# Performance work log

Measured on AMD Instinct MI355X. Metric: run time of the kernel, lower is better.

The kernel has to match this reference:

```python
import jax, jax.numpy as jnp
import numpy as np

N = 100000   # nodes
E = 3200000  # edges per graph
D = 16       # embedding_size, num_heads = 1
ATTN_SLOPE = 0.2   # DGL GATv2Conv negative_slope default
ACT_SLOPE = 0.01   # torch.nn.functional.leaky_relu default (activation arg)


def gatv2_layer(h, src, dst, W_src, b_src, W_dst, b_dst, attn):
    """DGL GATv2Conv with num_heads=1, activation=leaky_relu.
    h: [N, D]; src/dst: [E] int; W_*: [D, D]; b_*: [D]; attn: [D].
    """
    feat_src = h @ W_src + b_src          # [N, D]
    feat_dst = h @ W_dst + b_dst          # [N, D]
    el = feat_src[src]                    # [E, D] gather to edges
    e = jax.nn.leaky_relu(el + feat_dst[dst], ATTN_SLOPE)  # [E, D]
    score = e @ attn                      # [E] attention logits
    # segment softmax over incoming edges of each destination node
    smax = jax.ops.segment_max(score, dst, num_segments=N)
    smax = jnp.where(jnp.isfinite(smax), smax, 0.0)  # empty segments -> 0
    ex = jnp.exp(score - smax[dst])       # [E]
    denom = jax.ops.segment_sum(ex, dst, num_segments=N)  # [N]
    alpha = ex / denom[dst]               # [E]
    rst = jax.ops.segment_sum(alpha[:, None] * el, dst, num_segments=N)  # [N, D]
    return jax.nn.leaky_relu(rst, ACT_SLOPE)


def setup_inputs() -> dict:
    key = jax.random.key(0)
    ks = jax.random.split(key, 16)
    s = 1.0 / np.sqrt(D)
    return {
        "embedding": jax.random.normal(ks[0], (N, D), jnp.float32),
        "src1": jax.random.randint(ks[1], (E,), 0, N, jnp.int32),
        "dst1": jax.random.randint(ks[2], (E,), 0, N, jnp.int32),
        "src2": jax.random.randint(ks[3], (E,), 0, N, jnp.int32),
        "dst2": jax.random.randint(ks[4], (E,), 0, N, jnp.int32),
        "W_src1": jax.random.normal(ks[5], (D, D), jnp.float32) * s,
        "b_src1": jnp.zeros((D,), jnp.float32),
        "W_dst1": jax.random.normal(ks[6], (D, D), jnp.float32) * s,
        "b_dst1": jnp.zeros((D,), jnp.float32),
        "attn1": jax.random.normal(ks[7], (D,), jnp.float32) * s,
        "W_src2": jax.random.normal(ks[8], (D, D), jnp.float32) * s,
        "b_src2": jnp.zeros((D,), jnp.float32),
        "W_dst2": jax.random.normal(ks[9], (D, D), jnp.float32) * s,
        "b_dst2": jnp.zeros((D,), jnp.float32),
        "attn2": jax.random.normal(ks[10], (D,), jnp.float32) * s,
    }


def reference(embedding, src1, dst1, src2, dst2,
              W_src1, b_src1, W_dst1, b_dst1, attn1,
              W_src2, b_src2, W_dst2, b_dst2, attn2):
    user2item = gatv2_layer(embedding, src1, dst1, W_src1, b_src1, W_dst1, b_dst1, attn1)
    item_influence = gatv2_layer(user2item, src2, dst2, W_src2, b_src2, W_dst2, b_dst2, attn2)
    return item_influence  # [N, D]
```

## Files before the change

kernel.cpp:

```cpp
#include <hip/hip_runtime.h>
#include <hip/hip_fp16.h>

#define D 16
#define R 64
#define RBITS 6
#define RMASK 63
#define STRIDE 2560
#define CAP 2560
#define ACCT 512
#define KPT (CAP / ACCT)
#define EPB 16384
#define CHK 8192
#define K1T 1024
#define NB2 1664
#define ATTN_SLOPE 0.2f
#define ACT_SLOPE 0.01f

__device__ __forceinline__ float leaky_a(float v) {
    return v > 0.f ? v : ATTN_SLOPE * v;
}
__device__ __forceinline__ float2 h2f(unsigned u) {
    __half2 h = *(__half2*)&u;
    return __half22float2(h);
}


__device__ void binscatter_tile(int tile, const int* __restrict__ src,
                                const int* __restrict__ dst,
                                int* __restrict__ gcur, unsigned* __restrict__ binned,
                                int E, int NB, char* sb) {
    unsigned* sorted = (unsigned*)sb;
    unsigned short* sposb = (unsigned short*)(sb + 32768);
    int* soffs = (int*)(sb + 49152);
    int* wcur = (int*)(sb + 49152 + 4 * NB2);
    int* swsum = (int*)(sb + 49152 + 8 * NB2);
    int tid = threadIdx.x;
    int lane = tid & 63, w = tid >> 6;
    int base = tile * EPB;
    int count = E - base;
    if (count > EPB) count = EPB;

    for (int i = tid; i < NB; i += K1T) wcur[i] = 0;
    __syncthreads();

    if (count == EPB) {
        const int4* d4 = (const int4*)(dst + base);
#pragma unroll
        for (int m = 0; m < 4; m++) {
            int4 a = d4[m * K1T + tid];
            atomicAdd(&wcur[a.x >> RBITS], 1);
            atomicAdd(&wcur[a.y >> RBITS], 1);
            atomicAdd(&wcur[a.z >> RBITS], 1);
            atomicAdd(&wcur[a.w >> RBITS], 1);
        }
    } else {
        for (int k = 0; k < 16; k++) {
            int e = base + k * K1T + tid;
            if (e < E) atomicAdd(&wcur[dst[e] >> RBITS], 1);
        }
    }
    __syncthreads();

    for (int i = tid; i < NB; i += K1T) {
        int c = wcur[i];
        if (c > 0) {
            int res = atomicAdd(&gcur[i], c);
            wcur[i] = i * STRIDE + res;
        }
    }
    __syncthreads();

    int i0 = 2 * tid, i1 = 2 * tid + 1;
    for (int c = 0; c < 2; c++) {
        int cbase = base + c * CHK;
        int cc = count - c * CHK;
        if (cc <= 0) break;
        if (cc > CHK) cc = CHK;
        bool full = (cc == CHK);

        for (int i = tid; i < NB; i += K1T) soffs[i] = 0;
        __syncthreads();

        if (full) {
            const int4* d4 = (const int4*)(dst + cbase);
            int4 a = d4[tid], b4 = d4[K1T + tid];
            atomicAdd(&soffs[a.x >> RBITS], 1);
            atomicAdd(&soffs[a.y >> RBITS], 1);
            atomicAdd(&soffs[a.z >> RBITS], 1);
            atomicAdd(&soffs[a.w >> RBITS], 1);
            atomicAdd(&soffs[b4.x >> RBITS], 1);
            atomicAdd(&soffs[b4.y >> RBITS], 1);
            atomicAdd(&soffs[b4.z >> RBITS], 1);
            atomicAdd(&soffs[b4.w >> RBITS], 1);
        } else {
            for (int k = 0; k < 8; k++) {
                int e = cbase + k * K1T + tid;
                if (e < E) atomicAdd(&soffs[dst[e] >> RBITS], 1);
            }
        }
        __syncthreads();

        int a0 = (i0 < NB) ? soffs[i0] : 0;
        int a1 = (i1 < NB) ? soffs[i1] : 0;
        int pair = a0 + a1;
        int x = pair;
#pragma unroll
        for (int ofs = 1; ofs < 64; ofs <<= 1) {
            int y = __shfl_up(x, ofs, 64);
            if (lane >= ofs) x += y;
        }
        if (lane == 63) swsum[w] = x;
        __syncthreads();
        if (w == 0) {
            int v = (lane < 16) ? swsum[lane] : 0;
            int s = v;
#pragma unroll
            for (int ofs = 1; ofs < 16; ofs <<= 1) {
                int y = __shfl_up(s, ofs, 64);
                if (lane >= ofs) s += y;
            }
            if (lane < 16) swsum[lane] = s - v;
        }
        __syncthreads();
        int excl = x - pair + swsum[w];
        int e0 = excl, e1 = excl + a0;
        int d0v = 0, d1v = 0;
        if (i0 < NB) {
            soffs[i0] = e0;
            if (a0 > 0) { d0v = wcur[i0] - e0; wcur[i0] = d0v; }
        }
        if (i1 < NB) {
            soffs[i1] = e1;
            if (a1 > 0) { d1v = wcur[i1] - e1; wcur[i1] = d1v; }
        }
        __syncthreads();

        if (full) {
            const int4* d4 = (const int4*)(dst + cbase);
            const int4* s4 = (const int4*)(src + cbase);
            int4 a = d4[tid], b4 = d4[K1T + tid];
            int4 sa = s4[tid], sb4 = s4[K1T + tid];
            int dd[8] = {a.x, a.y, a.z, a.w, b4.x, b4.y, b4.z, b4.w};
            int ss[8] = {sa.x, sa.y, sa.z, sa.w, sb4.x, sb4.y, sb4.z, sb4.w};
#pragma unroll
            for (int m = 0; m < 8; m++) {
                int bb = dd[m] >> RBITS;
                int r = atomicAdd(&soffs[bb], 1);
                sorted[r] = ((unsigned)ss[m] << RBITS) | (unsigned)(dd[m] & RMASK);
                sposb[r] = (unsigned short)bb;
            }
        } else {
            for (int k = 0; k < 8; k++) {
                int e = cbase + k * K1T + tid;
                if (e < E) {
                    int dv = dst[e];
                    int bb = dv >> RBITS;
                    int r = atomicAdd(&soffs[bb], 1);
                    sorted[r] = ((unsigned)src[e] << RBITS) | (unsigned)(dv & RMASK);
                    sposb[r] = (unsigned short)bb;
                }
            }
        }
        __syncthreads();

#pragma unroll
        for (int m = 0; m < 8; m++) {
            int p = m * K1T + tid;
            if (p < cc) {
                int bb = sposb[p];
                int pos = p + wcur[bb];
                if (pos < (bb + 1) * STRIDE) binned[pos] = sorted[p];
            }
        }
        __syncthreads();

        if (c == 0) {
            if (i0 < NB && a0 > 0) wcur[i0] = d0v + e0 + a0;
            if (i1 < NB && a1 > 0) wcur[i1] = d1v + e1 + a1;
            __syncthreads();
        }
    }
}

__device__ void transform_tile(int tile, const float* __restrict__ h,
                               const float* __restrict__ Ws, const float* __restrict__ bs,
                               const float* __restrict__ Wd, const float* __restrict__ bd,
                               __half* __restrict__ fsh, float* __restrict__ fdst,
                               int N, char* sb) {
    float* sWs = (float*)sb;
    float* sWd = sWs + 256;
    float* sbs = sWd + 256;
    float* sbd = sbs + 16;
    int t = threadIdx.x;
    if (t < 256) { sWs[t] = Ws[t]; sWd[t] = Wd[t]; }
    if (t < 16) { sbs[t] = bs[t]; sbd[t] = bd[t]; }
    __syncthreads();
    int n = tile * K1T + t;
    if (n >= N) return;
    float hv[D];
    const float4* h4 = (const float4*)(h + (size_t)n * D);
#pragma unroll
    for (int k = 0; k < 4; k++) {
        float4 v = h4[k];
        hv[4 * k] = v.x; hv[4 * k + 1] = v.y; hv[4 * k + 2] = v.z; hv[4 * k + 3] = v.w;
    }
    float os[D], od[D];
#pragma unroll
    for (int d = 0; d < D; d++) {
        float ss = sbs[d];
        float sd = sbd[d];
#pragma unroll
        for (int k = 0; k < D; k++) {
            ss += hv[k] * sWs[k * D + d];
            sd += hv[k] * sWd[k * D + d];
        }
        os[d] = ss; od[d] = sd;
    }
    unsigned us[8];
#pragma unroll
    for (int k = 0; k < 8; k++) {
        __half2 hh = __floats2half2_rn(os[2 * k], os[2 * k + 1]);
        us[k] = *(unsigned*)&hh;
    }
    uint4* fo = (uint4*)(fsh + (size_t)n * D);
    fo[0] = make_uint4(us[0], us[1], us[2], us[3]);
    fo[1] = make_uint4(us[4], us[5], us[6], us[7]);
    float4* fd4 = (float4*)(fdst + (size_t)n * D);
#pragma unroll
    for (int k = 0; k < 4; k++)
        fd4[k] = make_float4(od[4 * k], od[4 * k + 1], od[4 * k + 2], od[4 * k + 3]);
}

__global__ void __launch_bounds__(K1T)
k1_kernel(const float* h, const float* Ws, const float* bs,
          const float* Wd, const float* bd,
          __half* fsh, float* fdst,
          const int* srcA, const int* dstA, int* gA, unsigned* binnedA, int EA,
          const int* srcB, const int* dstB, int* gB, unsigned* binnedB, int EB,
          int N, int NB, int B1, int B2, int TT) {
    __shared__ __align__(16) char sb[49152 + 8 * NB2 + 64];
    int bid = blockIdx.x;
    if (bid < B1) {
        binscatter_tile(bid, srcA, dstA, gA, binnedA, EA, NB, sb);
    } else if (bid < B1 + B2) {
        binscatter_tile(bid - B1, srcB, dstB, gB, binnedB, EB, NB, sb);
    } else {
        int t = bid - B1 - B2;
        if (t < TT) transform_tile(t, h, Ws, bs, Wd, bd, fsh, fdst, N, sb);
    }
}


template <bool DO_TAIL>
__global__ void __launch_bounds__(ACCT)
acc_kernel(const unsigned* __restrict__ binned, const int* __restrict__ gcur,
           const __half* __restrict__ fsh, const float* __restrict__ fdst,
           const float* __restrict__ attn, float* __restrict__ out,
           __half* __restrict__ fs2h, float* __restrict__ fd2,
           const float* __restrict__ Ws2, const float* __restrict__ bs2,
           const float* __restrict__ Wd2, const float* __restrict__ bd2,
           int N) {
    __shared__ float sfd[R * D];
    __shared__ int ebuf[CAP];
    __shared__ float exbuf[CAP];
    __shared__ int cstart[R + 1];
    __shared__ int cur[R];
    __shared__ float wtail[544];
    int b = blockIdx.x;
    int tid = threadIdx.x;
    int node0 = b * R;
    int nn = N - node0;
    if (nn > R) nn = R;
    for (int i = tid; i < nn * D; i += ACCT) sfd[i] = fdst[node0 * D + i];
    if (tid <= R) cstart[tid] = 0;
    if (DO_TAIL) {
        if (tid < 256) { wtail[tid] = Ws2[tid]; wtail[256 + tid] = Wd2[tid]; }
        if (tid < 16) { wtail[512 + tid] = bs2[tid]; wtail[528 + tid] = bd2[tid]; }
    }

    float av[D];
#pragma unroll
    for (int k = 0; k < D; k++) av[k] = attn[k];

    int cnt = gcur[b];
    if (cnt > CAP) cnt = CAP;
    int base = b * STRIDE;

    unsigned pls[KPT];
#pragma unroll
    for (int k = 0; k < KPT; k++) {
        int j = k * ACCT + tid;
        pls[k] = (j < cnt) ? binned[base + j] : 0xFFFFFFFFu;
    }
    __syncthreads();

    const uint4* fsh4 = (const uint4*)fsh;
    const uint2* fsq = (const uint2*)fsh;
    const float4* sfd4 = (const float4*)sfd;

#pragma unroll
    for (int k = 0; k < KPT; k++)
        if (pls[k] != 0xFFFFFFFFu) atomicAdd(&cstart[pls[k] & RMASK], 1);

    float exs[KPT];
#pragma unroll
    for (int k = 0; k + 1 < KPT; k += 2) {
        unsigned q0 = pls[k], q1 = pls[k + 1];
        uint4 ua0, ub0, ua1, ub1;
        if (q0 != 0xFFFFFFFFu) {
            int s = q0 >> RBITS;
            ua0 = fsh4[2 * s]; ub0 = fsh4[2 * s + 1];
        }
        if (q1 != 0xFFFFFFFFu) {
            int s = q1 >> RBITS;
            ua1 = fsh4[2 * s]; ub1 = fsh4[2 * s + 1];
        }
        if (q0 != 0xFFFFFFFFu) {
            int loc = q0 & RMASK;
            float4 f0 = sfd4[loc * 4 + 0], f1 = sfd4[loc * 4 + 1];
            float4 f2 = sfd4[loc * 4 + 2], f3 = sfd4[loc * 4 + 3];
            float2 c0 = h2f(ua0.x), c1 = h2f(ua0.y), c2 = h2f(ua0.z), c3 = h2f(ua0.w);
            float2 c4 = h2f(ub0.x), c5 = h2f(ub0.y), c6 = h2f(ub0.z), c7 = h2f(ub0.w);
            float p = leaky_a(c0.x + f0.x) * av[0]  + leaky_a(c0.y + f0.y) * av[1]
                    + leaky_a(c1.x + f0.z) * av[2]  + leaky_a(c1.y + f0.w) * av[3]
                    + leaky_a(c2.x + f1.x) * av[4]  + leaky_a(c2.y + f1.y) * av[5]
                    + leaky_a(c3.x + f1.z) * av[6]  + leaky_a(c3.y + f1.w) * av[7]
                    + leaky_a(c4.x + f2.x) * av[8]  + leaky_a(c4.y + f2.y) * av[9]
                    + leaky_a(c5.x + f2.z) * av[10] + leaky_a(c5.y + f2.w) * av[11]
                    + leaky_a(c6.x + f3.x) * av[12] + leaky_a(c6.y + f3.y) * av[13]
                    + leaky_a(c7.x + f3.z) * av[14] + leaky_a(c7.y + f3.w) * av[15];
            exs[k] = __expf(p);
        }
        if (q1 != 0xFFFFFFFFu) {
            int loc = q1 & RMASK;
            float4 f0 = sfd4[loc * 4 + 0], f1 = sfd4[loc * 4 + 1];
            float4 f2 = sfd4[loc * 4 + 2], f3 = sfd4[loc * 4 + 3];
            float2 c0 = h2f(ua1.x), c1 = h2f(ua1.y), c2 = h2f(ua1.z), c3 = h2f(ua1.w);
            float2 c4 = h2f(ub1.x), c5 = h2f(ub1.y), c6 = h2f(ub1.z), c7 = h2f(ub1.w);
            float p = leaky_a(c0.x + f0.x) * av[0]  + leaky_a(c0.y + f0.y) * av[1]
                    + leaky_a(c1.x + f0.z) * av[2]  + leaky_a(c1.y + f0.w) * av[3]
                    + leaky_a(c2.x + f1.x) * av[4]  + leaky_a(c2.y + f1.y) * av[5]
                    + leaky_a(c3.x + f1.z) * av[6]  + leaky_a(c3.y + f1.w) * av[7]
                    + leaky_a(c4.x + f2.x) * av[8]  + leaky_a(c4.y + f2.y) * av[9]
                    + leaky_a(c5.x + f2.z) * av[10] + leaky_a(c5.y + f2.w) * av[11]
                    + leaky_a(c6.x + f3.x) * av[12] + leaky_a(c6.y + f3.y) * av[13]
                    + leaky_a(c7.x + f3.z) * av[14] + leaky_a(c7.y + f3.w) * av[15];
            exs[k + 1] = __expf(p);
        }
    }
    if (KPT & 1) {
        unsigned q0 = pls[KPT - 1];
        if (q0 != 0xFFFFFFFFu) {
            int s = q0 >> RBITS;
            uint4 ua0 = fsh4[2 * s], ub0 = fsh4[2 * s + 1];
            int loc = q0 & RMASK;
            float4 f0 = sfd4[loc * 4 + 0], f1 = sfd4[loc * 4 + 1];
            float4 f2 = sfd4[loc * 4 + 2], f3 = sfd4[loc * 4 + 3];
            float2 c0 = h2f(ua0.x), c1 = h2f(ua0.y), c2 = h2f(ua0.z), c3 = h2f(ua0.w);
            float2 c4 = h2f(ub0.x), c5 = h2f(ub0.y), c6 = h2f(ub0.z), c7 = h2f(ub0.w);
            float p = leaky_a(c0.x + f0.x) * av[0]  + leaky_a(c0.y + f0.y) * av[1]
                    + leaky_a(c1.x + f0.z) * av[2]  + leaky_a(c1.y + f0.w) * av[3]
                    + leaky_a(c2.x + f1.x) * av[4]  + leaky_a(c2.y + f1.y) * av[5]
                    + leaky_a(c3.x + f1.z) * av[6]  + leaky_a(c3.y + f1.w) * av[7]
                    + leaky_a(c4.x + f2.x) * av[8]  + leaky_a(c4.y + f2.y) * av[9]
                    + leaky_a(c5.x + f2.z) * av[10] + leaky_a(c5.y + f2.w) * av[11]
                    + leaky_a(c6.x + f3.x) * av[12] + leaky_a(c6.y + f3.y) * av[13]
                    + leaky_a(c7.x + f3.z) * av[14] + leaky_a(c7.y + f3.w) * av[15];
            exs[KPT - 1] = __expf(p);
        }
    }
    __syncthreads();
    if (tid < R) {
        int v = cstart[tid];
        int x = v;
#pragma unroll
        for (int ofs = 1; ofs < 64; ofs <<= 1) {
            int y = __shfl_up(x, ofs, 64);
            if (tid >= ofs) x += y;
        }
        cstart[tid] = x - v;
        cur[tid] = x - v;
        if (tid == R - 1) cstart[R] = x;
    }
    __syncthreads();
#pragma unroll
    for (int k = 0; k < KPT; k++) {
        unsigned pl = pls[k];
        if (pl != 0xFFFFFFFFu) {
            int r = atomicAdd(&cur[pl & RMASK], 1);
            ebuf[r] = (int)pl;
            exbuf[r] = exs[k];
        }
    }
    __syncthreads();

    int lane = tid & 63;
    int w = tid >> 6;
    int q = lane & 3;
    int s2 = (lane >> 2) & 3;
    int n2 = lane >> 4;

    float4 acc[2];
    float den[2];
#pragma unroll
    for (int i = 0; i < 2; i++) {
        acc[i] = make_float4(0.f, 0.f, 0.f, 0.f);
        den[i] = 0.f;
    }
#pragma unroll
    for (int i = 0; i < 2; i++) {
        int loc = w * 8 + i * 4 + n2;
        int kb = cstart[loc], ke = cstart[loc + 1];
        int k = kb + s2;
        for (; k + 12 < ke; k += 16) {
            int pl0 = ebuf[k];
            int pl1 = ebuf[k + 4];
            int pl2 = ebuf[k + 8];
            int pl3 = ebuf[k + 12];
            float ex0 = exbuf[k];
            float ex1 = exbuf[k + 4];
            float ex2 = exbuf[k + 8];
            float ex3 = exbuf[k + 12];
            uint2 u0 = fsq[(((unsigned)pl0) >> RBITS) * 4 + q];
            uint2 u1 = fsq[(((unsigned)pl1) >> RBITS) * 4 + q];
            uint2 u2 = fsq[(((unsigned)pl2) >> RBITS) * 4 + q];
            uint2 u3 = fsq[(((unsigned)pl3) >> RBITS) * 4 + q];
            float2 a01 = h2f(u0.x), a23 = h2f(u0.y);
            float2 b01 = h2f(u1.x), b23 = h2f(u1.y);
            float2 c01 = h2f(u2.x), c23 = h2f(u2.y);
            float2 d01 = h2f(u3.x), d23 = h2f(u3.y);
            acc[i].x += ex0 * a01.x + ex1 * b01.x + ex2 * c01.x + ex3 * d01.x;
            acc[i].y += ex0 * a01.y + ex1 * b01.y + ex2 * c01.y + ex3 * d01.y;
            acc[i].z += ex0 * a23.x + ex1 * b23.x + ex2 * c23.x + ex3 * d23.x;
            acc[i].w += ex0 * a23.y + ex1 * b23.y + ex2 * c23.y + ex3 * d23.y;
            den[i] += (ex0 + ex1) + (ex2 + ex3);
        }
        for (; k < ke; k += 4) {
            int pl = ebuf[k];
            float ex = exbuf[k];
            uint2 u = fsq[(((unsigned)pl) >> RBITS) * 4 + q];
            float2 a01 = h2f(u.x), a23 = h2f(u.y);
            acc[i].x += ex * a01.x;
            acc[i].y += ex * a01.y;
            acc[i].z += ex * a23.x;
            acc[i].w += ex * a23.y;
            den[i] += ex;
        }
    }
#pragma unroll
    for (int i = 0; i < 2; i++) {
        float4 a = acc[i];
        float dn = den[i];
#pragma unroll
        for (int m = 4; m <= 8; m <<= 1) {
            a.x += __shfl_xor(a.x, m, 16);
            a.y += __shfl_xor(a.y, m, 16);
            a.z += __shfl_xor(a.z, m, 16);
            a.w += __shfl_xor(a.w, m, 16);
            dn += __shfl_xor(dn, m, 16);
        }
        int loc = w * 8 + i * 4 + n2;
        if (s2 == 0 && loc < nn) {
            float inv = dn > 0.f ? 1.f / dn : 0.f;
            float4 v;
            v.x = a.x * inv; v.x = v.x > 0.f ? v.x : ACT_SLOPE * v.x;
            v.y = a.y * inv; v.y = v.y > 0.f ? v.y : ACT_SLOPE * v.y;
            v.z = a.z * inv; v.z = v.z > 0.f ? v.z : ACT_SLOPE * v.z;
            v.w = a.w * inv; v.w = v.w > 0.f ? v.w : ACT_SLOPE * v.w;
            if (DO_TAIL) {
                *(float4*)&sfd[loc * D + q * 4] = v;
            } else {
                ((float4*)out)[(size_t)(node0 + loc) * 4 + q] = v;
            }
        }
    }
    if (DO_TAIL) {
        __syncthreads();
        int loc = tid >> 2, qq = tid & 3;
        if (tid < 256 && loc < nn) {
            float hvv[16];
#pragma unroll
            for (int k = 0; k < 16; k++) hvv[k] = sfd[loc * D + k];
            float s0 = wtail[512 + 4 * qq], s1 = wtail[513 + 4 * qq];
            float s2v = wtail[514 + 4 * qq], s3 = wtail[515 + 4 * qq];
            float d0 = wtail[528 + 4 * qq], d1 = wtail[529 + 4 * qq];
            float d2v = wtail[530 + 4 * qq], d3 = wtail[531 + 4 * qq];
#pragma unroll
            for (int k = 0; k < 16; k++) {
                float hk = hvv[k];
                const float* wr = &wtail[k * 16 + 4 * qq];
                const float* wr2 = &wtail[256 + k * 16 + 4 * qq];
                s0 += hk * wr[0]; s1 += hk * wr[1]; s2v += hk * wr[2]; s3 += hk * wr[3];
                d0 += hk * wr2[0]; d1 += hk * wr2[1]; d2v += hk * wr2[2]; d3 += hk * wr2[3];
            }
            __half2 p0 = __floats2half2_rn(s0, s1), p1 = __floats2half2_rn(s2v, s3);
            *(uint2*)(fs2h + (size_t)(node0 + loc) * D + 4 * qq) =
                make_uint2(*(unsigned*)&p0, *(unsigned*)&p1);
            *(float4*)(fd2 + (size_t)(node0 + loc) * D + 4 * qq) =
                make_float4(d0, d1, d2v, d3);
        }
    }
}


extern "C" void kernel_launch(void* const* d_in, const int* in_sizes, int n_in,
                              void* d_out, int out_size, void* d_ws, size_t ws_size,
                              hipStream_t stream) {
    const float* emb = (const float*)d_in[0];
    const int* src1 = (const int*)d_in[1];
    const int* dst1 = (const int*)d_in[2];
    const int* src2 = (const int*)d_in[3];
    const int* dst2 = (const int*)d_in[4];
    const float* Wsrc1 = (const float*)d_in[5];
    const float* bsrc1 = (const float*)d_in[6];
    const float* Wdst1 = (const float*)d_in[7];
    const float* bdst1 = (const float*)d_in[8];
    const float* attn1 = (const float*)d_in[9];
    const float* Wsrc2 = (const float*)d_in[10];
    const float* bsrc2 = (const float*)d_in[11];
    const float* Wdst2 = (const float*)d_in[12];
    const float* bdst2 = (const float*)d_in[13];
    const float* attn2 = (const float*)d_in[14];

    const int N = in_sizes[0] / D;
    const int E1 = in_sizes[1];
    const int E2 = in_sizes[3];
    const int NB = (N + R - 1) / R;
    const size_t ndf = (size_t)N * D;

    float* ws = (float*)d_ws;
    float* fd1 = ws;
    float* fd2 = fd1 + ndf;
    __half* fs1h = (__half*)(fd2 + ndf);
    __half* fs2h = fs1h + ndf;
    int* gA = (int*)(fs2h + ndf);
    int* gB = gA + NB2;
    unsigned* binned1 = (unsigned*)(gB + NB2);
    unsigned* binned2big = binned1 + (size_t)NB * STRIDE;
    size_t bigNeed = (size_t)((char*)(binned2big + (size_t)NB * STRIDE) - (char*)d_ws);
    bool big = ws_size >= bigNeed;
    (void)n_in; (void)out_size;

    const int B1 = (E1 + EPB - 1) / EPB;
    const int B2 = (E2 + EPB - 1) / EPB;
    const int TT = (N + K1T - 1) / K1T;

    (void)hipMemsetAsync(gA, 0, 2 * NB2 * sizeof(int), stream);

    if (big) {
        k1_kernel<<<B1 + B2 + TT, K1T, 0, stream>>>(
            emb, Wsrc1, bsrc1, Wdst1, bdst1, fs1h, fd1,
            src1, dst1, gA, binned1, E1,
            src2, dst2, gB, binned2big, E2,
            N, NB, B1, B2, TT);
        acc_kernel<true><<<NB, ACCT, 0, stream>>>(
            binned1, gA, fs1h, fd1, attn1, nullptr,
            fs2h, fd2, Wsrc2, bsrc2, Wdst2, bdst2, N);
        acc_kernel<false><<<NB, ACCT, 0, stream>>>(
            binned2big, gB, fs2h, fd2, attn2, (float*)d_out,
            nullptr, nullptr, nullptr, nullptr, nullptr, nullptr, N);
    } else {
        k1_kernel<<<B1 + TT, K1T, 0, stream>>>(
            emb, Wsrc1, bsrc1, Wdst1, bdst1, fs1h, fd1,
            src1, dst1, gA, binned1, E1,
            src2, dst2, gB, binned1, 0,
            N, NB, B1, 0, TT);
        acc_kernel<true><<<NB, ACCT, 0, stream>>>(
            binned1, gA, fs1h, fd1, attn1, nullptr,
            fs2h, fd2, Wsrc2, bsrc2, Wdst2, bdst2, N);
        k1_kernel<<<B2, K1T, 0, stream>>>(
            emb, Wsrc1, bsrc1, Wdst1, bdst1, fs1h, fd1,
            src2, dst2, gB, binned1, E2,
            src2, dst2, gB, binned1, 0,
            N, NB, B2, 0, 0);
        acc_kernel<false><<<NB, ACCT, 0, stream>>>(
            binned1, gB, fs2h, fd2, attn2, (float*)d_out,
            nullptr, nullptr, nullptr, nullptr, nullptr, nullptr, N);
    }
}
```

Baseline: 235.2 us.

## Replace per-node edge sort with shared-memory atomic accumulation of weighted features

The accumulation kernel no longer builds per-destination edge lists in shared memory (counting, prefix scan, scatter, then a second gather pass). Each thread now computes the softmax weight for its edges and adds the weighted source features plus the weight directly into a padded 17-float per-node accumulator using shared-memory float atomics. The score loop is also software-pipelined to prefetch the next edge's source features. This removes the second global gather and several block barriers, but adds 17 shared atomics per edge that contend when many edges share a destination, and makes the summation order nondeterministic.

```diff
diff --git a/kernel.cpp b/kernel.cpp
--- a/kernel.cpp
+++ b/kernel.cpp
@@ -13,6 +13,7 @@
 #define CHK 8192
 #define K1T 1024
 #define NB2 1664
+#define NW 17
 #define ATTN_SLOPE 0.2f
 #define ACT_SLOPE 0.01f
 
@@ -261,10 +262,7 @@
            const float* __restrict__ Wd2, const float* __restrict__ bd2,
            int N) {
     __shared__ float sfd[R * D];
-    __shared__ int ebuf[CAP];
-    __shared__ float exbuf[CAP];
-    __shared__ int cstart[R + 1];
-    __shared__ int cur[R];
+    __shared__ float num[R * NW];
     __shared__ float wtail[544];
     int b = blockIdx.x;
     int tid = threadIdx.x;
@@ -272,7 +270,7 @@
     int nn = N - node0;
     if (nn > R) nn = R;
     for (int i = tid; i < nn * D; i += ACCT) sfd[i] = fdst[node0 * D + i];
-    if (tid <= R) cstart[tid] = 0;
+    for (int i = tid; i < R * NW; i += ACCT) num[i] = 0.f;
     if (DO_TAIL) {
         if (tid < 256) { wtail[tid] = Ws2[tid]; wtail[256 + tid] = Wd2[tid]; }
         if (tid < 16) { wtail[512 + tid] = bs2[tid]; wtail[528 + tid] = bd2[tid]; }
@@ -295,32 +293,28 @@
     __syncthreads();
 
     const uint4* fsh4 = (const uint4*)fsh;
-    const uint2* fsq = (const uint2*)fsh;
     const float4* sfd4 = (const float4*)sfd;
 
-#pragma unroll
-    for (int k = 0; k < KPT; k++)
-        if (pls[k] != 0xFFFFFFFFu) atomicAdd(&cstart[pls[k] & RMASK], 1);
-
-    float exs[KPT];
-#pragma unroll
-    for (int k = 0; k + 1 < KPT; k += 2) {
-        unsigned q0 = pls[k], q1 = pls[k + 1];
-        uint4 ua0, ub0, ua1, ub1;
-        if (q0 != 0xFFFFFFFFu) {
-            int s = q0 >> RBITS;
-            ua0 = fsh4[2 * s]; ub0 = fsh4[2 * s + 1];
-        }
-        if (q1 != 0xFFFFFFFFu) {
-            int s = q1 >> RBITS;
-            ua1 = fsh4[2 * s]; ub1 = fsh4[2 * s + 1];
-        }
-        if (q0 != 0xFFFFFFFFu) {
-            int loc = q0 & RMASK;
+    unsigned qc = pls[0];
+    uint4 ua, ub;
+    if (qc != 0xFFFFFFFFu) {
+        int s = qc >> RBITS;
+        ua = fsh4[2 * s]; ub = fsh4[2 * s + 1];
+    }
+#pragma unroll
+    for (int k = 0; k < KPT; k++) {
+        unsigned qn = (k + 1 < KPT) ? pls[k + 1] : 0xFFFFFFFFu;
+        uint4 na, nb4;
+        if (qn != 0xFFFFFFFFu) {
+            int s = qn >> RBITS;
+            na = fsh4[2 * s]; nb4 = fsh4[2 * s + 1];
+        }
+        if (qc != 0xFFFFFFFFu) {
+            int loc = qc & RMASK;
             float4 f0 = sfd4[loc * 4 + 0], f1 = sfd4[loc * 4 + 1];
             float4 f2 = sfd4[loc * 4 + 2], f3 = sfd4[loc * 4 + 3];
-            float2 c0 = h2f(ua0.x), c1 = h2f(ua0.y), c2 = h2f(ua0.z), c3 = h2f(ua0.w);
-            float2 c4 = h2f(ub0.x), c5 = h2f(ub0.y), c6 = h2f(ub0.z), c7 = h2f(ub0.w);
+            float2 c0 = h2f(ua.x), c1 = h2f(ua.y), c2 = h2f(ua.z), c3 = h2f(ua.w);
+            float2 c4 = h2f(ub.x), c5 = h2f(ub.y), c6 = h2f(ub.z), c7 = h2f(ub.w);
             float p = leaky_a(c0.x + f0.x) * av[0]  + leaky_a(c0.y + f0.y) * av[1]
                     + leaky_a(c1.x + f0.z) * av[2]  + leaky_a(c1.y + f0.w) * av[3]
                     + leaky_a(c2.x + f1.x) * av[4]  + leaky_a(c2.y + f1.y) * av[5]
@@ -329,144 +323,33 @@
                     + leaky_a(c5.x + f2.z) * av[10] + leaky_a(c5.y + f2.w) * av[11]
                     + leaky_a(c6.x + f3.x) * av[12] + leaky_a(c6.y + f3.y) * av[13]
                     + leaky_a(c7.x + f3.z) * av[14] + leaky_a(c7.y + f3.w) * av[15];
-            exs[k] = __expf(p);
-        }
-        if (q1 != 0xFFFFFFFFu) {
-            int loc = q1 & RMASK;
-            float4 f0 = sfd4[loc * 4 + 0], f1 = sfd4[loc * 4 + 1];
-            float4 f2 = sfd4[loc * 4 + 2], f3 = sfd4[loc * 4 + 3];
-            float2 c0 = h2f(ua1.x), c1 = h2f(ua1.y), c2 = h2f(ua1.z), c3 = h2f(ua1.w);
-            float2 c4 = h2f(ub1.x), c5 = h2f(ub1.y), c6 = h2f(ub1.z), c7 = h2f(ub1.w);
-            float p = leaky_a(c0.x + f0.x) * av[0]  + leaky_a(c0.y + f0.y) * av[1]
-                    + leaky_a(c1.x + f0.z) * av[2]  + leaky_a(c1.y + f0.w) * av[3]
-                    + leaky_a(c2.x + f1.x) * av[4]  + leaky_a(c2.y + f1.y) * av[5]
-                    + leaky_a(c3.x + f1.z) * av[6]  + leaky_a(c3.y + f1.w) * av[7]
-                    + leaky_a(c4.x + f2.x) * av[8]  + leaky_a(c4.y + f2.y) * av[9]
-                    + leaky_a(c5.x + f2.z) * av[10] + leaky_a(c5.y + f2.w) * av[11]
-                    + leaky_a(c6.x + f3.x) * av[12] + leaky_a(c6.y + f3.y) * av[13]
-                    + leaky_a(c7.x + f3.z) * av[14] + leaky_a(c7.y + f3.w) * av[15];
-            exs[k + 1] = __expf(p);
-        }
-    }
-    if (KPT & 1) {
-        unsigned q0 = pls[KPT - 1];
-        if (q0 != 0xFFFFFFFFu) {
-            int s = q0 >> RBITS;
-            uint4 ua0 = fsh4[2 * s], ub0 = fsh4[2 * s + 1];
-            int loc = q0 & RMASK;
-            float4 f0 = sfd4[loc * 4 + 0], f1 = sfd4[loc * 4 + 1];
-            float4 f2 = sfd4[loc * 4 + 2], f3 = sfd4[loc * 4 + 3];
-            float2 c0 = h2f(ua0.x), c1 = h2f(ua0.y), c2 = h2f(ua0.z), c3 = h2f(ua0.w);
-            float2 c4 = h2f(ub0.x), c5 = h2f(ub0.y), c6 = h2f(ub0.z), c7 = h2f(ub0.w);
-            float p = leaky_a(c0.x + f0.x) * av[0]  + leaky_a(c0.y + f0.y) * av[1]
-                    + leaky_a(c1.x + f0.z) * av[2]  + leaky_a(c1.y + f0.w) * av[3]
-                    + leaky_a(c2.x + f1.x) * av[4]  + leaky_a(c2.y + f1.y) * av[5]
-                    + leaky_a(c3.x + f1.z) * av[6]  + leaky_a(c3.y + f1.w) * av[7]
-                    + leaky_a(c4.x + f2.x) * av[8]  + leaky_a(c4.y + f2.y) * av[9]
-                    + leaky_a(c5.x + f2.z) * av[10] + leaky_a(c5.y + f2.w) * av[11]
-                    + leaky_a(c6.x + f3.x) * av[12] + leaky_a(c6.y + f3.y) * av[13]
-                    + leaky_a(c7.x + f3.z) * av[14] + leaky_a(c7.y + f3.w) * av[15];
-            exs[KPT - 1] = __expf(p);
-        }
-    }
-    __syncthreads();
-    if (tid < R) {
-        int v = cstart[tid];
-        int x = v;
-#pragma unroll
-        for (int ofs = 1; ofs < 64; ofs <<= 1) {
-            int y = __shfl_up(x, ofs, 64);
-            if (tid >= ofs) x += y;
-        }
-        cstart[tid] = x - v;
-        cur[tid] = x - v;
-        if (tid == R - 1) cstart[R] = x;
-    }
-    __syncthreads();
-#pragma unroll
-    for (int k = 0; k < KPT; k++) {
-        unsigned pl = pls[k];
-        if (pl != 0xFFFFFFFFu) {
-            int r = atomicAdd(&cur[pl & RMASK], 1);
-            ebuf[r] = (int)pl;
-            exbuf[r] = exs[k];
-        }
-    }
-    __syncthreads();
-
-    int lane = tid & 63;
-    int w = tid >> 6;
-    int q = lane & 3;
-    int s2 = (lane >> 2) & 3;
-    int n2 = lane >> 4;
-
-    float4 acc[2];
-    float den[2];
-#pragma unroll
-    for (int i = 0; i < 2; i++) {
-        acc[i] = make_float4(0.f, 0.f, 0.f, 0.f);
-        den[i] = 0.f;
-    }
-#pragma unroll
-    for (int i = 0; i < 2; i++) {
-        int loc = w * 8 + i * 4 + n2;
-        int kb = cstart[loc], ke = cstart[loc + 1];
-        int k = kb + s2;
-        for (; k + 12 < ke; k += 16) {
-            int pl0 = ebuf[k];
-            int pl1 = ebuf[k + 4];
-            int pl2 = ebuf[k + 8];
-            int pl3 = ebuf[k + 12];
-            float ex0 = exbuf[k];
-            float ex1 = exbuf[k + 4];
-            float ex2 = exbuf[k + 8];
-            float ex3 = exbuf[k + 12];
-            uint2 u0 = fsq[(((unsigned)pl0) >> RBITS) * 4 + q];
-            uint2 u1 = fsq[(((unsigned)pl1) >> RBITS) * 4 + q];
-            uint2 u2 = fsq[(((unsigned)pl2) >> RBITS) * 4 + q];
-            uint2 u3 = fsq[(((unsigned)pl3) >> RBITS) * 4 + q];
-            float2 a01 = h2f(u0.x), a23 = h2f(u0.y);
-            float2 b01 = h2f(u1.x), b23 = h2f(u1.y);
-            float2 c01 = h2f(u2.x), c23 = h2f(u2.y);
-            float2 d01 = h2f(u3.x), d23 = h2f(u3.y);
-            acc[i].x += ex0 * a01.x + ex1 * b01.x + ex2 * c01.x + ex3 * d01.x;
-            acc[i].y += ex0 * a01.y + ex1 * b01.y + ex2 * c01.y + ex3 * d01.y;
-            acc[i].z += ex0 * a23.x + ex1 * b23.x + ex2 * c23.x + ex3 * d23.x;
-            acc[i].w += ex0 * a23.y + ex1 * b23.y + ex2 * c23.y + ex3 * d23.y;
-            den[i] += (ex0 + ex1) + (ex2 + ex3);
-        }
-        for (; k < ke; k += 4) {
-            int pl = ebuf[k];
-            float ex = exbuf[k];
-            uint2 u = fsq[(((unsigned)pl) >> RBITS) * 4 + q];
-            float2 a01 = h2f(u.x), a23 = h2f(u.y);
-            acc[i].x += ex * a01.x;
-            acc[i].y += ex * a01.y;
-            acc[i].z += ex * a23.x;
-            acc[i].w += ex * a23.y;
-            den[i] += ex;
-        }
-    }
-#pragma unroll
-    for (int i = 0; i < 2; i++) {
-        float4 a = acc[i];
-        float dn = den[i];
-#pragma unroll
-        for (int m = 4; m <= 8; m <<= 1) {
-            a.x += __shfl_xor(a.x, m, 16);
-            a.y += __shfl_xor(a.y, m, 16);
-            a.z += __shfl_xor(a.z, m, 16);
-            a.w += __shfl_xor(a.w, m, 16);
-            dn += __shfl_xor(dn, m, 16);
-        }
-        int loc = w * 8 + i * 4 + n2;
-        if (s2 == 0 && loc < nn) {
+            float ex = __expf(p);
+            float* nb = &num[loc * NW];
+            atomicAdd(&nb[16], ex);
+            atomicAdd(&nb[0],  ex * c0.x);  atomicAdd(&nb[1],  ex * c0.y);
+            atomicAdd(&nb[2],  ex * c1.x);  atomicAdd(&nb[3],  ex * c1.y);
+            atomicAdd(&nb[4],  ex * c2.x);  atomicAdd(&nb[5],  ex * c2.y);
+            atomicAdd(&nb[6],  ex * c3.x);  atomicAdd(&nb[7],  ex * c3.y);
+            atomicAdd(&nb[8],  ex * c4.x);  atomicAdd(&nb[9],  ex * c4.y);
+            atomicAdd(&nb[10], ex * c5.x);  atomicAdd(&nb[11], ex * c5.y);
+            atomicAdd(&nb[12], ex * c6.x);  atomicAdd(&nb[13], ex * c6.y);
+            atomicAdd(&nb[14], ex * c7.x);  atomicAdd(&nb[15], ex * c7.y);
+        }
+        qc = qn; ua = na; ub = nb4;
+    }
+    __syncthreads();
+
+    if (tid < 256) {
+        int loc = tid >> 2, q = tid & 3;
+        if (loc < nn) {
+            float dn = num[loc * NW + 16];
             float inv = dn > 0.f ? 1.f / dn : 0.f;
+            const float* nb = &num[loc * NW + q * 4];
             float4 v;
-            v.x = a.x * inv; v.x = v.x > 0.f ? v.x : ACT_SLOPE * v.x;
-            v.y = a.y * inv; v.y = v.y > 0.f ? v.y : ACT_SLOPE * v.y;
-            v.z = a.z * inv; v.z = v.z > 0.f ? v.z : ACT_SLOPE * v.z;
-            v.w = a.w * inv; v.w = v.w > 0.f ? v.w : ACT_SLOPE * v.w;
+            v.x = nb[0] * inv; v.x = v.x > 0.f ? v.x : ACT_SLOPE * v.x;
+            v.y = nb[1] * inv; v.y = v.y > 0.f ? v.y : ACT_SLOPE * v.y;
+            v.z = nb[2] * inv; v.z = v.z > 0.f ? v.z : ACT_SLOPE * v.z;
+            v.w = nb[3] * inv; v.w = v.w > 0.f ? v.w : ACT_SLOPE * v.w;
             if (DO_TAIL) {
                 *(float4*)&sfd[loc * D + q * 4] = v;
             } else {
```

After: 807.1 us. 3.43x slower.
